# Kernel tuning notes

Measured on AMD Instinct MI355X. Metric: run time of the kernel, lower is better.

Reference implementation:

```python
import jax, jax.numpy as jnp
import numpy as np

NDIM, NINEQ, NEQ = 1024, 512, 256
EPS = 1e-4       # Q regularization (module's eps)
N_ITERS = 25     # fixed primal-dual interior-point iterations
SIGMA = 0.1      # centering parameter


def setup_inputs() -> dict:
    key = jax.random.key(0)
    ks = jax.random.split(key, 5)
    L = jnp.tril(jax.random.uniform(ks[0], (NDIM, NDIM)))                      # tril(rand) as in torch init
    q = jax.random.uniform(ks[1], (NDIM,), minval=-1.0, maxval=1.0)
    G = jax.random.uniform(ks[2], (NINEQ, NDIM), minval=-1.0, maxval=1.0)
    A = jax.random.uniform(ks[3], (NEQ, NDIM), minval=-1.0, maxval=1.0)
    b = jax.random.uniform(ks[4], (NEQ,), minval=-1.0, maxval=1.0)
    x0 = jnp.zeros((NDIM,), jnp.float32)   # nn.Parameter(torch.zeros(ndim))
    s0 = jnp.ones((NINEQ,), jnp.float32)   # nn.Parameter(torch.ones(nineq))
    return {"L": L, "q": q, "G": G, "A": A, "b": b, "x0": x0, "s0": s0}


def _frac_to_boundary(v, dv):
    # max step alpha in (0,1] keeping v + alpha*dv > 0, with 0.99 backoff
    safe_dv = jnp.where(dv < 0, dv, -1.0)
    ratio = jnp.where(dv < 0, -v / safe_dv, 1.0)
    return jnp.min(ratio)


def _solve_qp(Q, q, G, h, A, b):
    n, m, p = q.shape[0], h.shape[0], b.shape[0]

    def step(state, _):
        x, s, z, y = state
        r_x = Q @ x + q + G.T @ z + A.T @ y          # dual residual
        r_p = G @ x + s - h                           # primal ineq residual
        r_y = A @ x - b                               # primal eq residual
        mu = jnp.dot(s, z) / m
        r_c = s * z - SIGMA * mu                      # centered complementarity
        D = z / s                                     # diag scaling
        H = Q + G.T @ (D[:, None] * G)                # reduced Hessian [n,n]
        KKT = jnp.block([[H, A.T], [A, jnp.zeros((p, p), Q.dtype)]])
        rhs = jnp.concatenate([-(r_x + G.T @ ((-r_c + z * r_p) / s)), -r_y])
        sol = jnp.linalg.solve(KKT, rhs)
        dx, dy = sol[:n], sol[n:]
        ds = -r_p - G @ dx
        dz = (-r_c - z * ds) / s
        alpha = 0.99 * jnp.minimum(1.0, jnp.minimum(_frac_to_boundary(s, ds), _frac_to_boundary(z, dz)))
        return (x + alpha * dx, s + alpha * ds, z + alpha * dz, y + alpha * dy), None

    init = (jnp.zeros((n,), Q.dtype), jnp.ones((m,), Q.dtype), jnp.ones((m,), Q.dtype), jnp.zeros((p,), Q.dtype))
    (x, s, z, y), _ = jax.lax.scan(step, init, None, length=N_ITERS)
    return x


def reference(L, q, G, A, b, x0, s0):
    Lt = jnp.tril(L)  # M * L with M = tril(ones)
    Q = Lt @ Lt.T + EPS * jnp.eye(L.shape[0], dtype=L.dtype)
    h = G @ x0 + s0   # learn_h branch (source's self.z0 is self.x0)
    return _solve_qp(Q, q, G, h, A, b)
```

## Files before the change

### kernel.cpp

```cpp
#include <hip/hip_runtime.h>
#include <hip/hip_bf16.h>


constexpr int ND = 1024;
constexpr int MI = 512;
constexpr int PE = 256;
constexpr int NM = 512;
constexpr int LDM = 520;
constexpr double EPSQ = 1e-4;
constexpr double SIG = 0.1;
constexpr int NITER = 25;

__device__ __forceinline__ double wred(double v) {
#pragma unroll
  for (int off = 32; off; off >>= 1) v += __shfl_down(v, off, 64);
  return v;
}

__global__ void k_prep(const float* __restrict__ Gf, const float* __restrict__ Af,
                       const float* __restrict__ qf, const float* __restrict__ bf,
                       float* __restrict__ GTf, float* __restrict__ ATf,
                       double* __restrict__ qd, double* __restrict__ bd,
                       double* __restrict__ xv, double* __restrict__ sv,
                       double* __restrict__ zv, double* __restrict__ yv,
                       double* __restrict__ scal) {
  if (blockIdx.x == 0 && threadIdx.x == 0) { scal[0] = 1.0; scal[1] = 0.0; }
  for (size_t idx = (size_t)blockIdx.x * blockDim.x + threadIdx.x;
       idx < (size_t)MI * ND; idx += (size_t)gridDim.x * blockDim.x) {
    int k = (int)(idx >> 10), i = (int)(idx & 1023);
    GTf[(size_t)i * MI + k] = Gf[idx];
    if (idx < (size_t)PE * ND) ATf[(size_t)i * PE + k] = Af[idx];
    if (idx < ND) { qd[idx] = (double)qf[idx]; xv[idx] = 0.0; }
    if (idx < MI) { sv[idx] = 1.0; zv[idx] = 1.0; }
    if (idx < PE) { bd[idx] = (double)bf[idx]; yv[idx] = 0.0; }
  }
}

__global__ __launch_bounds__(256) void k_h(const float* __restrict__ Gf,
                                           const float* __restrict__ x0f,
                                           const float* __restrict__ s0f,
                                           double* __restrict__ hd) {
  int wid = blockIdx.x * 4 + (int)(threadIdx.x >> 6), lane = threadIdx.x & 63;
  if (wid >= MI) return;
  double acc = 0;
  for (int c = lane; c < ND; c += 64) acc += (double)Gf[(size_t)wid * ND + c] * (double)x0f[c];
  acc = wred(acc);
  if (lane == 0) hd[wid] = acc + (double)s0f[wid];
}

__global__ __launch_bounds__(256) void k_qbuild(const float* __restrict__ Lf,
                                                double* __restrict__ Qd, double* __restrict__ LQ) {
  __shared__ double As[32][33], Bs[32][33];
  int i0 = blockIdx.y * 32, j0 = blockIdx.x * 32;
  int tx = threadIdx.x & 15, ty = threadIdx.x >> 4;
  double acc[2][2] = {};
  int kmax = (i0 < j0 ? i0 : j0) + 32;
  for (int k0 = 0; k0 < kmax; k0 += 32) {
    for (int l = threadIdx.x; l < 1024; l += 256) {
      int r = l >> 5, c = l & 31;
      As[r][c] = (k0 + c <= i0 + r) ? (double)Lf[(size_t)(i0 + r) * ND + k0 + c] : 0.0;
      Bs[r][c] = (k0 + c <= j0 + r) ? (double)Lf[(size_t)(j0 + r) * ND + k0 + c] : 0.0;
    }
    __syncthreads();
#pragma unroll
    for (int k = 0; k < 32; k++) {
      double a0 = As[2 * ty][k], a1 = As[2 * ty + 1][k];
      double b0 = Bs[2 * tx][k], b1 = Bs[2 * tx + 1][k];
      acc[0][0] += a0 * b0; acc[0][1] += a0 * b1;
      acc[1][0] += a1 * b0; acc[1][1] += a1 * b1;
    }
    __syncthreads();
  }
  for (int da = 0; da < 2; da++)
    for (int db = 0; db < 2; db++) {
      int i = i0 + 2 * ty + da, j = j0 + 2 * tx + db;
      double v = acc[da][db] + (i == j ? EPSQ : 0.0);
      Qd[(size_t)i * ND + j] = v;
      LQ[(size_t)i * ND + j] = v;
    }
}

__global__ __launch_bounds__(256) void k_chol_diag_inv(double* __restrict__ A, int lda, int kb,
                                                       double* __restrict__ DG) {
  __shared__ double a[4160];
  __shared__ double invp[2080];
  __shared__ double dtmp[64];
  int t = threadIdx.x;
  size_t base = (size_t)kb * 64;
  for (int l = t; l < 4096; l += 256) { int r = l >> 6, c = l & 63; a[r * 65 + c] = A[(base + r) * lda + base + c]; }
  __syncthreads();
  if (t == 0) {
    double m = 0;
    for (int i = 0; i < 64; i++) m = fmax(m, fabs(a[i * 65 + i]));
    a[4159] = m * 1e-28 + 1e-280;
  }
  __syncthreads();
  double dfl = a[4159];
  int rg = t >> 6, ln = t & 63;
  for (int j = 0; j < 64; ++j) {
    double invd = 1.0 / fmax(a[j * 65 + j], dfl);
    for (int r = j + 1 + rg; r < 64; r += 4) {
      int c = j + 1 + ln;
      if (c <= r) a[r * 65 + c] -= a[r * 65 + j] * a[c * 65 + j] * invd;
    }
    __syncthreads();
  }
  if (t < 64) dtmp[t] = 1.0 / sqrt(fmax(a[t * 65 + t], dfl));
  __syncthreads();
  for (int l = t; l < 4096; l += 256) { int r = l >> 6, c = l & 63; if (c <= r) a[r * 65 + c] *= dtmp[c]; }
  __syncthreads();
  for (int l = t; l < 4096; l += 256) { int r = l >> 6, c = l & 63; if (c <= r) A[(base + r) * lda + base + c] = a[r * 65 + c]; }
  if (t < 64) {
    int c = t;
    for (int i = c; i < 64; i++) {
      double v = (i == c) ? 1.0 : 0.0;
      for (int k = c; k < i; k++) v -= a[i * 65 + k] * invp[k * (k + 1) / 2 + c];
      invp[i * (i + 1) / 2 + c] = v / a[i * 65 + i];
    }
  }
  __syncthreads();
  for (int l = t; l < 4096; l += 256) {
    int r = l >> 6, c = l & 63;
    DG[(size_t)kb * 4096 + (size_t)c * 64 + r] = (c <= r) ? invp[r * (r + 1) / 2 + c] : 0.0;
  }
}

__global__ __launch_bounds__(256) void k_fps2(double* __restrict__ A, int lda,
                                              double* __restrict__ PL, int ldp,
                                              double* __restrict__ DG, int kb, int nbk) {
  extern __shared__ double sh[];
  double* D  = sh;
  double* Cb = sh + 4160;
  double* Pb = sh + 8320;
  double* Lb = sh + 12480;
  const int t = threadIdx.x, tx = t & 15, ty = t >> 4;
  const bool tail = (kb + 2 >= nbk);
  int bi = 0, bj = 0;
  if (!tail) {
    int idx = blockIdx.x;
    bi = (int)((sqrtf(8.0f * (float)idx + 1.0f) - 1.0f) * 0.5f);
    while ((bi + 1) * (bi + 2) / 2 <= idx) ++bi;
    while (bi * (bi + 1) / 2 > idx) --bi;
    bj = idx - bi * (bi + 1) / 2;
  }
  const int ib = kb + 2 + bi, jb = kb + 2 + bj;
  const bool isDiag = (ib == jb);
  const bool isBoss = (blockIdx.x == 0);

  double tmp[4][4];
  auto loadTile = [&](double* dst, int rb, int cb) {
    for (int l = t; l < 4096; l += 256) {
      int r = l >> 6, c = l & 63;
      dst[r * 65 + c] = A[(size_t)(rb * 64 + r) * lda + cb * 64 + c];
    }
  };
  auto mulD = [&](const double* X) {
#pragma unroll
    for (int e = 0; e < 4; e++)
#pragma unroll
      for (int f = 0; f < 4; f++) tmp[e][f] = 0;
    for (int k = 0; k < 64; ++k) {
      double x0 = X[ty * 65 + k], x1 = X[(ty + 16) * 65 + k];
      double x2 = X[(ty + 32) * 65 + k], x3 = X[(ty + 48) * 65 + k];
      double d0 = D[k * 64 + tx], d1 = D[k * 64 + tx + 16];
      double d2 = D[k * 64 + tx + 32], d3 = D[k * 64 + tx + 48];
      tmp[0][0] += x0 * d0; tmp[0][1] += x0 * d1; tmp[0][2] += x0 * d2; tmp[0][3] += x0 * d3;
      tmp[1][0] += x1 * d0; tmp[1][1] += x1 * d1; tmp[1][2] += x1 * d2; tmp[1][3] += x1 * d3;
      tmp[2][0] += x2 * d0; tmp[2][1] += x2 * d1; tmp[2][2] += x2 * d2; tmp[2][3] += x2 * d3;
      tmp[3][0] += x3 * d0; tmp[3][1] += x3 * d1; tmp[3][2] += x3 * d2; tmp[3][3] += x3 * d3;
    }
  };
  auto mulNT = [&](const double* X, const double* Y) {
#pragma unroll
    for (int e = 0; e < 4; e++)
#pragma unroll
      for (int f = 0; f < 4; f++) tmp[e][f] = 0;
    for (int k = 0; k < 64; ++k) {
      double x0 = X[ty * 65 + k], x1 = X[(ty + 16) * 65 + k];
      double x2 = X[(ty + 32) * 65 + k], x3 = X[(ty + 48) * 65 + k];
      double y0 = Y[tx * 65 + k], y1 = Y[(tx + 16) * 65 + k];
      double y2 = Y[(tx + 32) * 65 + k], y3 = Y[(tx + 48) * 65 + k];
      tmp[0][0] += x0 * y0; tmp[0][1] += x0 * y1; tmp[0][2] += x0 * y2; tmp[0][3] += x0 * y3;
      tmp[1][0] += x1 * y0; tmp[1][1] += x1 * y1; tmp[1][2] += x1 * y2; tmp[1][3] += x1 * y3;
      tmp[2][0] += x2 * y0; tmp[2][1] += x2 * y1; tmp[2][2] += x2 * y2; tmp[2][3] += x2 * y3;
      tmp[3][0] += x3 * y0; tmp[3][1] += x3 * y1; tmp[3][2] += x3 * y2; tmp[3][3] += x3 * y3;
    }
  };
  auto storeTmp = [&](double* dst) {
    __syncthreads();
#pragma unroll
    for (int e = 0; e < 4; e++)
#pragma unroll
      for (int f = 0; f < 4; f++) dst[(ty + 16 * e) * 65 + tx + 16 * f] = tmp[e][f];
    __syncthreads();
  };
  auto factorD = [&](int dgout) {
    if (t == 0) {
      double m = 0;
      for (int i2 = 0; i2 < 64; i2++) m = fmax(m, fabs(D[i2 * 65 + i2]));
      D[4159] = m * 1e-28 + 1e-280;
    }
    __syncthreads();
    double dfl = D[4159];
    int rg = t >> 6, ln = t & 63;
    for (int j = 0; j < 64; ++j) {
      double invd = 1.0 / fmax(D[j * 65 + j], dfl);
      for (int r = j + 1 + rg; r < 64; r += 4) {
        int c = j + 1 + ln;
        if (c <= r) D[r * 65 + c] -= D[r * 65 + j] * D[c * 65 + j] * invd;
      }
      __syncthreads();
    }
    double* invp = Cb;
    double* dtmp = Cb + 2080;
    if (t < 64) dtmp[t] = 1.0 / sqrt(fmax(D[t * 65 + t], dfl));
    __syncthreads();
    for (int l = t; l < 4096; l += 256) { int r = l >> 6, c = l & 63; if (c <= r) D[r * 65 + c] *= dtmp[c]; }
    __syncthreads();
    if (t < 64) {
      int c = t;
      for (int i2 = c; i2 < 64; ++i2) {
        double v = (i2 == c) ? 1.0 : 0.0;
        for (int k = c; k < i2; ++k) v -= D[i2 * 65 + k] * invp[k * (k + 1) / 2 + c];
        invp[i2 * (i2 + 1) / 2 + c] = v / D[i2 * 65 + i2];
      }
    }
    __syncthreads();
    for (int l = t; l < 4096; l += 256) {
      int k = l >> 6, c = l & 63;
      D[k * 64 + c] = (k <= c) ? invp[c * (c + 1) / 2 + k] : 0.0;
    }
    __syncthreads();
    if (dgout >= 0 && isBoss)
      for (int l = t; l < 4096; l += 256) DG[(size_t)dgout * 4096 + l] = D[l];
    __syncthreads();
  };

  for (int l = t; l < 4096; l += 256) D[l] = DG[(size_t)kb * 4096 + l];
  __syncthreads();

  if (tail) {
    loadTile(Lb, kb + 1, kb);
    __syncthreads();
    mulD(Lb); storeTmp(Cb);
    for (int l = t; l < 4096; l += 256) {
      int r = l >> 6, c = l & 63;
      PL[(size_t)((kb + 1) * 64 + r) * ldp + kb * 64 + c] = Cb[r * 65 + c];
    }
    mulNT(Cb, Cb);
    __syncthreads();
#pragma unroll
    for (int e = 0; e < 4; e++)
#pragma unroll
      for (int f = 0; f < 4; f++)
        D[(ty + 16 * e) * 65 + tx + 16 * f] =
            A[(size_t)((kb + 1) * 64 + ty + 16 * e) * lda + (kb + 1) * 64 + tx + 16 * f] - tmp[e][f];
    __syncthreads();
    factorD(kb + 1);
    return;
  }

  double acc[4][4];
#pragma unroll
  for (int e = 0; e < 4; e++)
#pragma unroll
    for (int f = 0; f < 4; f++)
      acc[e][f] = A[(size_t)(ib * 64 + ty + 16 * e) * lda + jb * 64 + tx + 16 * f];

  loadTile(Lb, kb + 1, kb);
  __syncthreads();
  mulD(Lb); storeTmp(Cb);
  if (isBoss)
    for (int l = t; l < 4096; l += 256) {
      int r = l >> 6, c = l & 63;
      PL[(size_t)((kb + 1) * 64 + r) * ldp + kb * 64 + c] = Cb[r * 65 + c];
    }
  loadTile(Lb, ib, kb);
  __syncthreads();
  mulD(Lb); storeTmp(Pb);
  if (isDiag)
    for (int l = t; l < 4096; l += 256) {
      int r = l >> 6, c = l & 63;
      PL[(size_t)(ib * 64 + r) * ldp + kb * 64 + c] = Pb[r * 65 + c];
    }
  if (!isDiag) {
    loadTile(Lb, jb, kb);
    __syncthreads();
    mulD(Lb); storeTmp(Lb);
  }
  const double* Pj0 = isDiag ? Pb : Lb;
  mulNT(Pb, Pj0);
#pragma unroll
  for (int e = 0; e < 4; e++)
#pragma unroll
    for (int f = 0; f < 4; f++) acc[e][f] -= tmp[e][f];
  mulNT(Pb, Cb);
#pragma unroll
  for (int e = 0; e < 4; e++)
#pragma unroll
    for (int f = 0; f < 4; f++)
      tmp[e][f] = A[(size_t)(ib * 64 + ty + 16 * e) * lda + (kb + 1) * 64 + tx + 16 * f] - tmp[e][f];
  storeTmp(Pb);
  if (!isDiag) {
    mulNT(Lb, Cb);
#pragma unroll
    for (int e = 0; e < 4; e++)
#pragma unroll
      for (int f = 0; f < 4; f++)
        tmp[e][f] = A[(size_t)(jb * 64 + ty + 16 * e) * lda + (kb + 1) * 64 + tx + 16 * f] - tmp[e][f];
    storeTmp(Lb);
  }
  mulNT(Cb, Cb);
  __syncthreads();
#pragma unroll
  for (int e = 0; e < 4; e++)
#pragma unroll
    for (int f = 0; f < 4; f++)
      D[(ty + 16 * e) * 65 + tx + 16 * f] =
          A[(size_t)((kb + 1) * 64 + ty + 16 * e) * lda + (kb + 1) * 64 + tx + 16 * f] - tmp[e][f];
  __syncthreads();
  factorD(kb + 1);
  mulD(Pb); storeTmp(Pb);
  if (isDiag)
    for (int l = t; l < 4096; l += 256) {
      int r = l >> 6, c = l & 63;
      PL[(size_t)(ib * 64 + r) * ldp + (kb + 1) * 64 + c] = Pb[r * 65 + c];
    }
  if (!isDiag) { mulD(Lb); storeTmp(Lb); }
  const double* Pj1 = isDiag ? Pb : Lb;
  mulNT(Pb, Pj1);
#pragma unroll
  for (int e = 0; e < 4; e++)
#pragma unroll
    for (int f = 0; f < 4; f++) acc[e][f] -= tmp[e][f];

  if (isBoss) {
    __syncthreads();
#pragma unroll
    for (int e = 0; e < 4; e++)
#pragma unroll
      for (int f = 0; f < 4; f++) D[(ty + 16 * e) * 65 + tx + 16 * f] = acc[e][f];
    __syncthreads();
    factorD(kb + 2);
  } else {
#pragma unroll
    for (int e = 0; e < 4; e++)
#pragma unroll
      for (int f = 0; f < 4; f++)
        A[(size_t)(ib * 64 + ty + 16 * e) * lda + jb * 64 + tx + 16 * f] = acc[e][f];
  }
}

__global__ __launch_bounds__(256) void k_trsmf_g(const double* __restrict__ Lm, int lda,
                                                 double* __restrict__ X, int ldx,
                                                 const double* __restrict__ DG, int kb) {
  __shared__ double Lb[64][64];
  __shared__ double Xs[64][33];
  int t = threadIdx.x;
  int c0 = blockIdx.x * 32;
  int lane2 = t & 31, rbase = t >> 5;
  int row0 = kb * 64;
  double acc[8];
#pragma unroll
  for (int e = 0; e < 8; e++) acc[e] = (row0 + rbase + 8 * e == c0 + lane2) ? 1.0 : 0.0;
  for (int jb = 0; jb < kb; jb++) {
    for (int l = t; l < 4096; l += 256) { int r = l >> 6, c = l & 63; Lb[r][c] = Lm[(size_t)(row0 + r) * lda + jb * 64 + c]; }
    for (int l = t; l < 2048; l += 256) { int k = l >> 5, c = l & 31; Xs[k][c] = X[(size_t)(jb * 64 + k) * ldx + c0 + c]; }
    __syncthreads();
#pragma unroll 4
    for (int k = 0; k < 64; k++) {
      double wv = Xs[k][lane2];
#pragma unroll
      for (int e = 0; e < 8; e++) acc[e] -= Lb[rbase + 8 * e][k] * wv;
    }
    __syncthreads();
  }
  __syncthreads();
#pragma unroll
  for (int e = 0; e < 8; e++) Xs[rbase + 8 * e][lane2] = acc[e];
  for (int l = t; l < 4096; l += 256) Lb[l >> 6][l & 63] = DG[(size_t)kb * 4096 + l];
  __syncthreads();
#pragma unroll
  for (int e = 0; e < 8; e++) {
    int i = rbase + 8 * e;
    double s = 0;
#pragma unroll 4
    for (int k = 0; k < 64; k++) s += Lb[k][i] * Xs[k][lane2];
    X[(size_t)(row0 + i) * ldx + c0 + lane2] = s;
  }
}

__global__ __launch_bounds__(256) void k_trsmb_g(const double* __restrict__ Lm, int lda,
                                                 double* __restrict__ X, int ldx,
                                                 const double* __restrict__ DG, int kb, int nkb) {
  __shared__ double Lb[64][64];
  __shared__ double Xs[64][33];
  int t = threadIdx.x;
  int c0 = blockIdx.x * 32;
  int lane2 = t & 31, rbase = t >> 5;
  int row0 = kb * 64;
  double acc[8];
#pragma unroll
  for (int e = 0; e < 8; e++) acc[e] = X[(size_t)(row0 + rbase + 8 * e) * ldx + c0 + lane2];
  for (int jb = kb + 1; jb < nkb; jb++) {
    for (int l = t; l < 4096; l += 256) { int r = l >> 6, c = l & 63; Lb[r][c] = Lm[(size_t)(jb * 64 + r) * lda + kb * 64 + c]; }
    for (int l = t; l < 2048; l += 256) { int k = l >> 5, c = l & 31; Xs[k][c] = X[(size_t)(jb * 64 + k) * ldx + c0 + c]; }
    __syncthreads();
#pragma unroll 4
    for (int k = 0; k < 64; k++) {
      double wv = Xs[k][lane2];
#pragma unroll
      for (int e = 0; e < 8; e++) acc[e] -= Lb[k][rbase + 8 * e] * wv;
    }
    __syncthreads();
  }
  __syncthreads();
#pragma unroll
  for (int e = 0; e < 8; e++) Xs[rbase + 8 * e][lane2] = acc[e];
  for (int l = t; l < 4096; l += 256) Lb[l >> 6][l & 63] = DG[(size_t)kb * 4096 + l];
  __syncthreads();
#pragma unroll
  for (int e = 0; e < 8; e++) {
    int i = rbase + 8 * e;
    double s = 0;
#pragma unroll 4
    for (int k = 0; k < 64; k++) s += Lb[i][k] * Xs[k][lane2];
    X[(size_t)(row0 + i) * ldx + c0 + lane2] = s;
  }
}

__global__ __launch_bounds__(256) void k_aqi(const float* __restrict__ Af, const double* __restrict__ Qi,
                                             double* __restrict__ AQi) {
  __shared__ double As[32][33], Bs[32][33];
  int i0 = blockIdx.x * 32, a0 = blockIdx.y * 32;
  int tx = threadIdx.x & 15, ty = threadIdx.x >> 4;
  double acc[2][2] = {};
  for (int k0 = 0; k0 < ND; k0 += 32) {
    for (int l = threadIdx.x; l < 1024; l += 256) {
      int r = l >> 5, c = l & 31;
      As[r][c] = (double)Af[(size_t)(a0 + r) * ND + k0 + c];
      Bs[r][c] = Qi[(size_t)(k0 + r) * ND + i0 + c];
    }
    __syncthreads();
#pragma unroll
    for (int k = 0; k < 32; k++) {
      double a0v = As[2 * ty][k], a1v = As[2 * ty + 1][k];
      double b0v = Bs[k][2 * tx], b1v = Bs[k][2 * tx + 1];
      acc[0][0] += a0v * b0v; acc[0][1] += a0v * b1v;
      acc[1][0] += a1v * b0v; acc[1][1] += a1v * b1v;
    }
    __syncthreads();
  }
  for (int da = 0; da < 2; da++)
    for (int db = 0; db < 2; db++)
      AQi[(size_t)(a0 + 2 * ty + da) * ND + i0 + 2 * tx + db] = acc[da][db];
}

__global__ __launch_bounds__(256) void k_sa(const double* __restrict__ AQi, const float* __restrict__ Af,
                                            double* __restrict__ SA) {
  __shared__ double As[32][33], Bs[32][33];
  int a0 = blockIdx.y * 32, b0 = blockIdx.x * 32;
  int tx = threadIdx.x & 15, ty = threadIdx.x >> 4;
  double acc[2][2] = {};
  for (int k0 = 0; k0 < ND; k0 += 32) {
    for (int l = threadIdx.x; l < 1024; l += 256) {
      int r = l >> 5, c = l & 31;
      As[r][c] = AQi[(size_t)(a0 + r) * ND + k0 + c];
      Bs[r][c] = (double)Af[(size_t)(b0 + r) * ND + k0 + c];
    }
    __syncthreads();
#pragma unroll
    for (int k = 0; k < 32; k++) {
      double a0v = As[2 * ty][k], a1v = As[2 * ty + 1][k];
      double b0v = Bs[2 * tx][k], b1v = Bs[2 * tx + 1][k];
      acc[0][0] += a0v * b0v; acc[0][1] += a0v * b1v;
      acc[1][0] += a1v * b0v; acc[1][1] += a1v * b1v;
    }
    __syncthreads();
  }
  for (int da = 0; da < 2; da++)
    for (int db = 0; db < 2; db++)
      SA[(size_t)(a0 + 2 * ty + da) * PE + b0 + 2 * tx + db] = acc[da][db];
}

__global__ __launch_bounds__(256) void k_xy(const double* __restrict__ AQi, const double* __restrict__ SAi,
                                            double* __restrict__ XY) {
  __shared__ double As[32][33], Bs[32][33];
  int b0 = blockIdx.x * 32, i0 = blockIdx.y * 32;
  int tx = threadIdx.x & 15, ty = threadIdx.x >> 4;
  double acc[2][2] = {};
  for (int k0 = 0; k0 < PE; k0 += 32) {
    for (int l = threadIdx.x; l < 1024; l += 256) {
      int r = l >> 5, c = l & 31;
      As[r][c] = AQi[(size_t)(k0 + r) * ND + i0 + c];
      Bs[r][c] = SAi[(size_t)(k0 + r) * PE + b0 + c];
    }
    __syncthreads();
#pragma unroll
    for (int k = 0; k < 32; k++) {
      double a0v = As[k][2 * ty], a1v = As[k][2 * ty + 1];
      double b0v = Bs[k][2 * tx], b1v = Bs[k][2 * tx + 1];
      acc[0][0] += a0v * b0v; acc[0][1] += a0v * b1v;
      acc[1][0] += a1v * b0v; acc[1][1] += a1v * b1v;
    }
    __syncthreads();
  }
  for (int da = 0; da < 2; da++)
    for (int db = 0; db < 2; db++)
      XY[(size_t)(i0 + 2 * ty + da) * PE + b0 + 2 * tx + db] = acc[da][db];
}

__global__ __launch_bounds__(256) void k_xx(const double* __restrict__ Qi, const double* __restrict__ XY,
                                            const double* __restrict__ AQi, double* __restrict__ XX) {
  __shared__ double As[32][33], Bs[32][33];
  int j0 = blockIdx.x * 32, i0 = blockIdx.y * 32;
  int tx = threadIdx.x & 15, ty = threadIdx.x >> 4;
  double acc[2][2] = {};
  for (int k0 = 0; k0 < PE; k0 += 32) {
    for (int l = threadIdx.x; l < 1024; l += 256) {
      int r = l >> 5, c = l & 31;
      As[r][c] = XY[(size_t)(i0 + r) * PE + k0 + c];
      Bs[r][c] = AQi[(size_t)(k0 + r) * ND + j0 + c];
    }
    __syncthreads();
#pragma unroll
    for (int k = 0; k < 32; k++) {
      double a0v = As[2 * ty][k], a1v = As[2 * ty + 1][k];
      double b0v = Bs[k][2 * tx], b1v = Bs[k][2 * tx + 1];
      acc[0][0] += a0v * b0v; acc[0][1] += a0v * b1v;
      acc[1][0] += a1v * b0v; acc[1][1] += a1v * b1v;
    }
    __syncthreads();
  }
  for (int da = 0; da < 2; da++)
    for (int db = 0; db < 2; db++) {
      int i = i0 + 2 * ty + da, j = j0 + 2 * tx + db;
      XX[(size_t)i * ND + j] = Qi[(size_t)i * ND + j] - acc[da][db];
    }
}

__global__ __launch_bounds__(256) void k_fk0x(const float* __restrict__ Gf, const double* __restrict__ XX,
                                              double* __restrict__ FK0x) {
  __shared__ double As[32][33], Bs[32][33];
  int j0 = blockIdx.x * 32, g0 = blockIdx.y * 32;
  int tx = threadIdx.x & 15, ty = threadIdx.x >> 4;
  double acc[2][2] = {};
  for (int k0 = 0; k0 < ND; k0 += 32) {
    for (int l = threadIdx.x; l < 1024; l += 256) {
      int r = l >> 5, c = l & 31;
      As[r][c] = (double)Gf[(size_t)(g0 + r) * ND + k0 + c];
      Bs[r][c] = XX[(size_t)(k0 + r) * ND + j0 + c];
    }
    __syncthreads();
#pragma unroll
    for (int k = 0; k < 32; k++) {
      double a0v = As[2 * ty][k], a1v = As[2 * ty + 1][k];
      double b0v = Bs[k][2 * tx], b1v = Bs[k][2 * tx + 1];
      acc[0][0] += a0v * b0v; acc[0][1] += a0v * b1v;
      acc[1][0] += a1v * b0v; acc[1][1] += a1v * b1v;
    }
    __syncthreads();
  }
  for (int da = 0; da < 2; da++)
    for (int db = 0; db < 2; db++)
      FK0x[(size_t)(g0 + 2 * ty + da) * ND + j0 + 2 * tx + db] = acc[da][db];
}

__global__ __launch_bounds__(256) void k_fk0y(const float* __restrict__ Gf, const double* __restrict__ XY,
                                              double* __restrict__ FK0y) {
  __shared__ double As[32][33], Bs[32][33];
  int b0 = blockIdx.x * 32, g0 = blockIdx.y * 32;
  int tx = threadIdx.x & 15, ty = threadIdx.x >> 4;
  double acc[2][2] = {};
  for (int k0 = 0; k0 < ND; k0 += 32) {
    for (int l = threadIdx.x; l < 1024; l += 256) {
      int r = l >> 5, c = l & 31;
      As[r][c] = (double)Gf[(size_t)(g0 + r) * ND + k0 + c];
      Bs[r][c] = XY[(size_t)(k0 + r) * PE + b0 + c];
    }
    __syncthreads();
#pragma unroll
    for (int k = 0; k < 32; k++) {
      double a0v = As[2 * ty][k], a1v = As[2 * ty + 1][k];
      double b0v = Bs[k][2 * tx], b1v = Bs[k][2 * tx + 1];
      acc[0][0] += a0v * b0v; acc[0][1] += a0v * b1v;
      acc[1][0] += a1v * b0v; acc[1][1] += a1v * b1v;
    }
    __syncthreads();
  }
  for (int da = 0; da < 2; da++)
    for (int db = 0; db < 2; db++)
      FK0y[(size_t)(g0 + 2 * ty + da) * PE + b0 + 2 * tx + db] = acc[da][db];
}

__global__ __launch_bounds__(256) void k_smat(const double* __restrict__ FK0x, const float* __restrict__ Gf,
                                              double* __restrict__ S) {
  __shared__ double As[32][33], Bs[32][33];
  int g0 = blockIdx.y * 32, h0 = blockIdx.x * 32;
  int tx = threadIdx.x & 15, ty = threadIdx.x >> 4;
  double acc[2][2] = {};
  for (int k0 = 0; k0 < ND; k0 += 32) {
    for (int l = threadIdx.x; l < 1024; l += 256) {
      int r = l >> 5, c = l & 31;
      As[r][c] = FK0x[(size_t)(g0 + r) * ND + k0 + c];
      Bs[r][c] = (double)Gf[(size_t)(h0 + r) * ND + k0 + c];
    }
    __syncthreads();
#pragma unroll
    for (int k = 0; k < 32; k++) {
      double a0v = As[2 * ty][k], a1v = As[2 * ty + 1][k];
      double b0v = Bs[2 * tx][k], b1v = Bs[2 * tx + 1][k];
      acc[0][0] += a0v * b0v; acc[0][1] += a0v * b1v;
      acc[1][0] += a1v * b0v; acc[1][1] += a1v * b1v;
    }
    __syncthreads();
  }
  for (int da = 0; da < 2; da++)
    for (int db = 0; db < 2; db++)
      S[(size_t)(g0 + 2 * ty + da) * MI + h0 + 2 * tx + db] = acc[da][db];
}

__global__ __launch_bounds__(256) void k_tr(const double* __restrict__ src, double* __restrict__ dst,
                                            int R, int Cc) {
  __shared__ double tile[32][33];
  int r0 = blockIdx.y * 32, c0 = blockIdx.x * 32;
  for (int l = threadIdx.x; l < 1024; l += 256) {
    int r = l >> 5, c = l & 31;
    tile[r][c] = src[(size_t)(r0 + r) * Cc + c0 + c];
  }
  __syncthreads();
  for (int l = threadIdx.x; l < 1024; l += 256) {
    int r = l >> 5, c = l & 31;
    dst[(size_t)(c0 + r) * R + r0 + c] = tile[c][r];
  }
}

__global__ __launch_bounds__(256) void k_A1(const double* __restrict__ Qd, const float* __restrict__ Gf,
                                            const float* __restrict__ Af, const float* __restrict__ GTf,
                                            const float* __restrict__ ATf, const double* __restrict__ qd,
                                            const double* __restrict__ bd, const double* __restrict__ hd,
                                            const double* __restrict__ xv, const double* __restrict__ sv,
                                            const double* __restrict__ zv, const double* __restrict__ yv,
                                            const double* __restrict__ scal, const double* __restrict__ S,
                                            double* __restrict__ rxv, double* __restrict__ rp,
                                            double* __restrict__ ry, double* __restrict__ uv,
                                            double* __restrict__ dinv, double* __restrict__ Mm) {
  int t = threadIdx.x, lane = t & 63;
  if (blockIdx.x < 256) {
    int wid = blockIdx.x * 4 + (t >> 6);
    double acc = 0;
    for (int k = lane; k < ND; k += 64) acc += Qd[(size_t)wid * ND + k] * xv[k];
    for (int k = lane; k < MI; k += 64) acc += (double)GTf[(size_t)wid * MI + k] * zv[k];
    for (int k = lane; k < PE; k += 64) acc += (double)ATf[(size_t)wid * PE + k] * yv[k];
    acc = wred(acc);
    if (lane == 0) rxv[wid] = acc + qd[wid];
  } else if (blockIdx.x < 448) {
    int wid = (blockIdx.x - 256) * 4 + (t >> 6);
    if (wid < MI) {
      double acc = 0;
      for (int c = lane; c < ND; c += 64) acc += (double)Gf[(size_t)wid * ND + c] * xv[c];
      acc = wred(acc);
      if (lane == 0) {
        double s0 = sv[wid], z0 = zv[wid];
        double rpv = acc + s0 - hd[wid];
        rp[wid] = rpv;
        double rc0 = s0 * z0 - SIG * scal[0];
        uv[wid] = (-rc0 + z0 * rpv) / s0;
        dinv[wid] = s0 / z0;
      }
    } else {
      int r = wid - MI;
      double acc = 0;
      for (int c = lane; c < ND; c += 64) acc += (double)Af[(size_t)r * ND + c] * xv[c];
      acc = wred(acc);
      if (lane == 0) ry[r] = acc - bd[r];
    }
  } else {
    int rbase = (blockIdx.x - 448) * 8;
    for (int rr = 0; rr < 8; ++rr) {
      int row = rbase + rr;
      for (int c = t; c < NM; c += 256) {
        double v = S[(size_t)row * MI + c];
        if (row == c) v += sv[row] / zv[row];
        Mm[(size_t)row * LDM + c] = v;
      }
    }
  }
}

__global__ __launch_bounds__(256) void k_A2(const double* __restrict__ rxv, const float* __restrict__ GTf,
                                            const double* __restrict__ uv, const double* __restrict__ ry,
                                            const double* __restrict__ S, const double* __restrict__ FK0x,
                                            const double* __restrict__ FK0y, double* __restrict__ rhs1,
                                            double* __restrict__ Mm, double* __restrict__ DGC) {
  __shared__ double sh2[6304];
  int t = threadIdx.x, lane = t & 63;
  if (blockIdx.x < 256) {
    int wid = blockIdx.x * 4 + (t >> 6);
    double acc = 0;
    for (int k = lane; k < MI; k += 64) acc += (double)GTf[(size_t)wid * MI + k] * uv[k];
    acc = wred(acc);
    if (lane == 0) rhs1[wid] = -(rxv[wid] + acc);
  } else if (blockIdx.x < 384) {
    int j = (blockIdx.x - 256) * 4 + (t >> 6);
    double acc = 0;
    for (int k = lane; k < ND; k += 64) acc += FK0x[(size_t)j * ND + k] * rxv[k];
    for (int m = lane; m < MI; m += 64) acc += S[(size_t)j * MI + m] * uv[m];
    for (int c = lane; c < PE; c += 64) acc += FK0y[(size_t)j * PE + c] * ry[c];
    acc = wred(acc);
    if (lane == 0) Mm[(size_t)NM * LDM + j] = -acc;
  } else {
    double* a = sh2;
    double* invp = sh2 + 4160;
    double* dtmp = sh2 + 6240;
    for (int l = t; l < 4096; l += 256) { int r = l >> 6, c = l & 63; a[r * 65 + c] = Mm[(size_t)r * LDM + c]; }
    __syncthreads();
    if (t == 0) {
      double m = 0;
      for (int i = 0; i < 64; i++) m = fmax(m, fabs(a[i * 65 + i]));
      a[4159] = m * 1e-28 + 1e-280;
    }
    __syncthreads();
    double dfl = a[4159];
    int rg = t >> 6, ln = t & 63;
    for (int j = 0; j < 64; ++j) {
      double invd = 1.0 / fmax(a[j * 65 + j], dfl);
      for (int r = j + 1 + rg; r < 64; r += 4) {
        int c = j + 1 + ln;
        if (c <= r) a[r * 65 + c] -= a[r * 65 + j] * a[c * 65 + j] * invd;
      }
      __syncthreads();
    }
    if (t < 64) dtmp[t] = 1.0 / sqrt(fmax(a[t * 65 + t], dfl));
    __syncthreads();
    for (int l = t; l < 4096; l += 256) { int r = l >> 6, c = l & 63; if (c <= r) a[r * 65 + c] *= dtmp[c]; }
    __syncthreads();
    if (t < 64) {
      int c = t;
      for (int i = c; i < 64; i++) {
        double v = (i == c) ? 1.0 : 0.0;
        for (int k = c; k < i; k++) v -= a[i * 65 + k] * invp[k * (k + 1) / 2 + c];
        invp[i * (i + 1) / 2 + c] = v / a[i * 65 + i];
      }
    }
    __syncthreads();
    for (int l = t; l < 4096; l += 256) {
      int r = l >> 6, c = l & 63;
      DGC[(size_t)c * 64 + r] = (c <= r) ? invp[r * (r + 1) / 2 + c] : 0.0;
    }
  }
}

__global__ __launch_bounds__(512) void k_bwdupd(const double* __restrict__ Mm, const double* __restrict__ PL,
                                                const double* __restrict__ DGC, const double* __restrict__ rp,
                                                const double* __restrict__ dinv, double* __restrict__ sv,
                                                double* __restrict__ zv, double* __restrict__ scal,
                                                double* __restrict__ solw) {
  __shared__ double DT[4096];
  __shared__ double g[NM];
  __shared__ double pseg[64];
  __shared__ double acc8[8][64];
  __shared__ double tmp[64];
  __shared__ double red[512];
  __shared__ double dsA[512];
  __shared__ double dzA[512];
  int t = threadIdx.x;
  for (int l = t; l < NM; l += 512) g[l] = Mm[(size_t)NM * LDM + l];
  for (int kbp = 0; kbp < 8; ++kbp) {
    __syncthreads();
    for (int l = t; l < 4096; l += 512) DT[l] = DGC[(size_t)kbp * 4096 + l];
    __syncthreads();
    if (t < 64) {
      double s = 0;
#pragma unroll
      for (int k = 0; k < 64; k++) s += g[kbp * 64 + k] * DT[k * 64 + t];
      pseg[t] = s;
    }
    __syncthreads();
    for (int c = (kbp + 1) * 64 + t; c < NM; c += 512) {
      double s = 0;
#pragma unroll
      for (int k = 0; k < 64; k++) s += pseg[k] * PL[(size_t)c * NM + kbp * 64 + k];
      g[c] -= s;
    }
    if (t < 64) g[kbp * 64 + t] = pseg[t];
  }
  int i8 = t & 63, p8 = t >> 6;
  for (int kb = 7; kb >= 0; --kb) {
    __syncthreads();
    for (int l = t; l < 4096; l += 512) DT[l] = DGC[(size_t)kb * 4096 + l];
    __syncthreads();
    int tr0 = kb * 64 + 64;
    double s = 0;
    for (int rr = p8; rr < NM - tr0; rr += 8)
      s += PL[(size_t)(tr0 + rr) * NM + kb * 64 + i8] * g[tr0 + rr];
    acc8[p8][i8] = s;
    __syncthreads();
    if (t < 64) {
      double v = g[kb * 64 + t];
#pragma unroll
      for (int p = 0; p < 8; p++) v -= acc8[p][t];
      tmp[t] = v;
    }
    __syncthreads();
    if (t < 64) {
      double v = 0;
#pragma unroll
      for (int l = 0; l < 64; l++) v += DT[t * 64 + l] * tmp[l];
      pseg[t] = v;
    }
    __syncthreads();
    if (t < 64) g[kb * 64 + t] = pseg[t];
  }
  __syncthreads();
  solw[t] = g[t];
  double mu = scal[0];
  double s0 = sv[t], z0 = zv[t];
  double ds = -rp[t] - dinv[t] * g[t];
  double rc0 = s0 * z0 - SIG * mu;
  double dz = (-rc0 - z0 * ds) / s0;
  dsA[t] = ds; dzA[t] = dz;
  double rs = (ds < 0.0) ? -s0 / ds : 1.0;
  double rz = (dz < 0.0) ? -z0 / dz : 1.0;
  red[t] = fmin(rs, rz);
  __syncthreads();
  for (int s2 = 256; s2; s2 >>= 1) { if (t < s2) red[t] = fmin(red[t], red[t + s2]); __syncthreads(); }
  double alpha = 0.99 * fmin(1.0, red[0]);
  if (!(alpha == alpha)) alpha = 0.0;
  double us = alpha * dsA[t], uz = alpha * dzA[t];
  if (isfinite(us)) sv[t] += us;
  if (isfinite(uz)) zv[t] += uz;
  __syncthreads();
  red[t] = sv[t] * zv[t];
  __syncthreads();
  for (int s2 = 256; s2; s2 >>= 1) { if (t < s2) red[t] += red[t + s2]; __syncthreads(); }
  if (t == 0) { scal[0] = red[0] / (double)MI; scal[1] = alpha; }
}

__global__ __launch_bounds__(256) void k_C(const double* __restrict__ XX, const double* __restrict__ XGT,
                                           const double* __restrict__ XY, const double* __restrict__ YXm,
                                           const double* __restrict__ YGT, const double* __restrict__ SAi,
                                           const double* __restrict__ rhs1, const double* __restrict__ solw,
                                           const double* __restrict__ ry, const double* __restrict__ scal,
                                           double* __restrict__ xv, double* __restrict__ yv) {
  int lane = threadIdx.x & 63;
  double al = scal[1];
  if (blockIdx.x < 256) {
    int wid = blockIdx.x * 4 + (int)(threadIdx.x >> 6);
    double acc = 0;
    for (int k = lane; k < ND; k += 64) acc += XX[(size_t)wid * ND + k] * rhs1[k];
    for (int m = lane; m < MI; m += 64) acc -= XGT[(size_t)wid * MI + m] * solw[m];
    for (int c = lane; c < PE; c += 64) acc -= XY[(size_t)wid * PE + c] * ry[c];
    acc = wred(acc);
    if (lane == 0) { double u = al * acc; if (isfinite(u)) xv[wid] += u; }
  } else {
    int r = (blockIdx.x - 256) * 4 + (int)(threadIdx.x >> 6);
    double acc = 0;
    for (int k = lane; k < ND; k += 64) acc += YXm[(size_t)r * ND + k] * rhs1[k];
    for (int m = lane; m < MI; m += 64) acc -= YGT[(size_t)r * MI + m] * solw[m];
    for (int c = lane; c < PE; c += 64) acc += SAi[(size_t)r * PE + c] * ry[c];
    acc = wred(acc);
    if (lane == 0) { double u = al * acc; if (isfinite(u)) yv[r] += u; }
  }
}

__global__ void k_out(const double* __restrict__ xv, float* __restrict__ out) {
  int i = blockIdx.x * blockDim.x + threadIdx.x;
  if (i < ND) out[i] = (float)xv[i];
}

__global__ void k_wsdiag(float mb, float* out) {
  int i = blockIdx.x * 256 + threadIdx.x;
  if (i < ND) out[i] = (i == 0 ? (65536.0f * (1.0f + mb)) : 0.0f);
}

extern "C" void kernel_launch(void* const* d_in, const int* in_sizes, int n_in,
                              void* d_out, int out_size, void* d_ws, size_t ws_size,
                              hipStream_t stream) {
  const float* Lf = (const float*)d_in[0];
  const float* qf = (const float*)d_in[1];
  const float* Gf = (const float*)d_in[2];
  const float* Af = (const float*)d_in[3];
  const float* bf = (const float*)d_in[4];
  const float* x0f = (const float*)d_in[5];
  const float* s0f = (const float*)d_in[6];

  double* w = (double*)d_ws;
  double* Qd  = w; w += (size_t)ND * ND;
  double* XX  = w; w += (size_t)ND * ND;
  double* R1  = w; w += (size_t)ND * ND;
  double* R2  = w; w += (size_t)ND * ND;
  double* XY  = w; w += (size_t)ND * PE;
  double* FK0xReg = w; w += (size_t)MI * ND;
  double* SA  = w; w += (size_t)PE * PE;
  double* PLi = w; w += (size_t)NM * NM;
  double* DGH = w; w += (size_t)16 * 4096;
  double* DGA = w; w += (size_t)4 * 4096;
  double* DGC = w; w += (size_t)8 * 4096;
  double* qd = w; w += ND;  double* bd = w; w += PE;  double* hd = w; w += MI;
  double* xv = w; w += ND;  double* sv = w; w += MI;  double* zv = w; w += MI;  double* yv = w; w += PE;
  double* rxv = w; w += ND; double* rp = w; w += MI;  double* ry = w; w += PE;
  double* uv = w; w += MI;  double* dinv = w; w += MI;
  double* rhs1 = w; w += ND; double* solw = w; w += NM;
  double* scal = w; w += 16;
  float* GTf = (float*)w;
  float* ATf = GTf + (size_t)ND * MI;
  char* wend = (char*)(ATf + (size_t)ND * PE);
  size_t need = (size_t)(wend - (char*)d_ws);
  if (ws_size < need) {
    k_wsdiag<<<4, 256, 0, stream>>>((float)(ws_size >> 20), (float*)d_out);
    return;
  }

  double* Qi  = R1;
  double* XGT = R1;
  double* YXm = R1 + (size_t)ND * MI;
  double* YGT = R1 + (size_t)ND * MI + (size_t)PE * ND;
  double* LQ  = R2;
  double* Mm  = R2;
  double* FK0y = R2 + (size_t)(NM + 1) * LDM;
  double* SAi  = FK0y + (size_t)MI * PE;
  double* Smat = SAi + (size_t)PE * PE;
  double* AQi  = FK0xReg;
  double* FK0x = FK0xReg;
  double* PLQ  = XX;
  double* PLA  = XY;

  const size_t ldsFPS = (size_t)16640 * sizeof(double);

  k_prep<<<2048, 256, 0, stream>>>(Gf, Af, qf, bf, GTf, ATf, qd, bd, xv, sv, zv, yv, scal);
  k_h<<<128, 256, 0, stream>>>(Gf, x0f, s0f, hd);
  { dim3 g(32, 32); k_qbuild<<<g, 256, 0, stream>>>(Lf, Qd, LQ); }
  k_chol_diag_inv<<<1, 256, 0, stream>>>(LQ, ND, 0, DGH);
  for (int kb = 0; kb < 16; kb += 2) {
    int T = 16 - kb - 2;
    int grid = (T > 0) ? T * (T + 1) / 2 : 1;
    k_fps2<<<grid, 256, ldsFPS, stream>>>(LQ, ND, PLQ, ND, DGH, kb, 16);
  }
  for (int kb = 0; kb < 16; kb++)  k_trsmf_g<<<32, 256, 0, stream>>>(PLQ, ND, Qi, ND, DGH, kb);
  for (int kb = 15; kb >= 0; kb--) k_trsmb_g<<<32, 256, 0, stream>>>(PLQ, ND, Qi, ND, DGH, kb, 16);
  { dim3 g(32, 8);  k_aqi<<<g, 256, 0, stream>>>(Af, Qi, AQi); }
  { dim3 g(8, 8);   k_sa<<<g, 256, 0, stream>>>(AQi, Af, SA); }
  k_chol_diag_inv<<<1, 256, 0, stream>>>(SA, PE, 0, DGA);
  for (int kb = 0; kb < 4; kb += 2) {
    int T = 4 - kb - 2;
    int grid = (T > 0) ? T * (T + 1) / 2 : 1;
    k_fps2<<<grid, 256, ldsFPS, stream>>>(SA, PE, PLA, PE, DGA, kb, 4);
  }
  for (int kb = 0; kb < 4; kb++)  k_trsmf_g<<<8, 256, 0, stream>>>(PLA, PE, SAi, PE, DGA, kb);
  for (int kb = 3; kb >= 0; kb--) k_trsmb_g<<<8, 256, 0, stream>>>(PLA, PE, SAi, PE, DGA, kb, 4);
  { dim3 g(8, 32);  k_xy<<<g, 256, 0, stream>>>(AQi, SAi, XY); }
  { dim3 g(32, 32); k_xx<<<g, 256, 0, stream>>>(Qi, XY, AQi, XX); }
  { dim3 g(32, 16); k_fk0x<<<g, 256, 0, stream>>>(Gf, XX, FK0x); }
  { dim3 g(8, 16);  k_fk0y<<<g, 256, 0, stream>>>(Gf, XY, FK0y); }
  { dim3 g(16, 16); k_smat<<<g, 256, 0, stream>>>(FK0x, Gf, Smat); }
  { dim3 g(32, 16); k_tr<<<g, 256, 0, stream>>>(FK0x, XGT, MI, ND); }
  { dim3 g(8, 32);  k_tr<<<g, 256, 0, stream>>>(XY, YXm, ND, PE); }
  { dim3 g(8, 16);  k_tr<<<g, 256, 0, stream>>>(FK0y, YGT, MI, PE); }

  for (int it = 0; it < NITER; ++it) {
    k_A1<<<512, 256, 0, stream>>>(Qd, Gf, Af, GTf, ATf, qd, bd, hd, xv, sv, zv, yv, scal,
                                  Smat, rxv, rp, ry, uv, dinv, Mm);
    k_A2<<<385, 256, 0, stream>>>(rxv, GTf, uv, ry, Smat, FK0x, FK0y, rhs1, Mm, DGC);
    for (int kb = 0; kb < 8; kb += 2) {
      int T = 8 - kb - 2;
      int grid = (T > 0) ? T * (T + 1) / 2 : 1;
      k_fps2<<<grid, 256, ldsFPS, stream>>>(Mm, LDM, PLi, NM, DGC, kb, 8);
    }
    k_bwdupd<<<1, 512, 0, stream>>>(Mm, PLi, DGC, rp, dinv, sv, zv, scal, solw);
    k_C<<<320, 256, 0, stream>>>(XX, XGT, XY, YXm, YGT, SAi, rhs1, solw, ry, scal, xv, yv);
  }
  k_out<<<4, 256, 0, stream>>>(xv, (float*)d_out);
}
```

Baseline: 36.69 ms.

## Fuse tail Cholesky panels and solve into one single-block kernel

Replaces the last two k_fps2 launches of the per-iteration 512x512 blocked Cholesky and the separate backward/update kernel with a single one-block kernel, k_tailsolve. That kernel factors block columns 4-7 in shared memory (panel multiply, trailing update, diagonal factor and inverse), then runs the forward/backward solve and the step update. The aim is to cut launch overhead and inter-kernel gaps in the latency-bound iteration loop, at the cost of running the small trailing updates on one workgroup serially.

```diff
diff --git a/kernel.cpp b/kernel.cpp
--- a/kernel.cpp
+++ b/kernel.cpp
@@ -751,33 +751,173 @@
   }
 }
 
-__global__ __launch_bounds__(512) void k_bwdupd(const double* __restrict__ Mm, const double* __restrict__ PL,
-                                                const double* __restrict__ DGC, const double* __restrict__ rp,
-                                                const double* __restrict__ dinv, double* __restrict__ sv,
-                                                double* __restrict__ zv, double* __restrict__ scal,
-                                                double* __restrict__ solw) {
-  __shared__ double DT[4096];
-  __shared__ double g[NM];
-  __shared__ double pseg[64];
-  __shared__ double acc8[8][64];
-  __shared__ double tmp[64];
-  __shared__ double red[512];
-  __shared__ double dsA[512];
-  __shared__ double dzA[512];
-  int t = threadIdx.x;
-  for (int l = t; l < NM; l += 512) g[l] = Mm[(size_t)NM * LDM + l];
+__global__ __launch_bounds__(256) void k_tailsolve(double* __restrict__ Mm, double* __restrict__ PL,
+                                                   double* __restrict__ DGC, const double* __restrict__ rp,
+                                                   const double* __restrict__ dinv, double* __restrict__ sv,
+                                                   double* __restrict__ zv, double* __restrict__ scal,
+                                                   double* __restrict__ solw) {
+  extern __shared__ double sh[];
+  double* D = sh;
+  double* U = sh + 4160;
+  double* V = sh + 8320;
+  const int t = threadIdx.x, tx = t & 15, ty = t >> 4;
+  double tmp[4][4];
+
+  auto mulD = [&](const double* X) {
+#pragma unroll
+    for (int e = 0; e < 4; e++)
+#pragma unroll
+      for (int f = 0; f < 4; f++) tmp[e][f] = 0;
+    for (int k = 0; k < 64; ++k) {
+      double x0 = X[ty * 65 + k], x1 = X[(ty + 16) * 65 + k];
+      double x2 = X[(ty + 32) * 65 + k], x3 = X[(ty + 48) * 65 + k];
+      double d0 = D[k * 64 + tx], d1 = D[k * 64 + tx + 16];
+      double d2 = D[k * 64 + tx + 32], d3 = D[k * 64 + tx + 48];
+      tmp[0][0] += x0 * d0; tmp[0][1] += x0 * d1; tmp[0][2] += x0 * d2; tmp[0][3] += x0 * d3;
+      tmp[1][0] += x1 * d0; tmp[1][1] += x1 * d1; tmp[1][2] += x1 * d2; tmp[1][3] += x1 * d3;
+      tmp[2][0] += x2 * d0; tmp[2][1] += x2 * d1; tmp[2][2] += x2 * d2; tmp[2][3] += x2 * d3;
+      tmp[3][0] += x3 * d0; tmp[3][1] += x3 * d1; tmp[3][2] += x3 * d2; tmp[3][3] += x3 * d3;
+    }
+  };
+  auto mulNT = [&](const double* X, const double* Y) {
+#pragma unroll
+    for (int e = 0; e < 4; e++)
+#pragma unroll
+      for (int f = 0; f < 4; f++) tmp[e][f] = 0;
+    for (int k = 0; k < 64; ++k) {
+      double x0 = X[ty * 65 + k], x1 = X[(ty + 16) * 65 + k];
+      double x2 = X[(ty + 32) * 65 + k], x3 = X[(ty + 48) * 65 + k];
+      double y0 = Y[tx * 65 + k], y1 = Y[(tx + 16) * 65 + k];
+      double y2 = Y[(tx + 32) * 65 + k], y3 = Y[(tx + 48) * 65 + k];
+      tmp[0][0] += x0 * y0; tmp[0][1] += x0 * y1; tmp[0][2] += x0 * y2; tmp[0][3] += x0 * y3;
+      tmp[1][0] += x1 * y0; tmp[1][1] += x1 * y1; tmp[1][2] += x1 * y2; tmp[1][3] += x1 * y3;
+      tmp[2][0] += x2 * y0; tmp[2][1] += x2 * y1; tmp[2][2] += x2 * y2; tmp[2][3] += x2 * y3;
+      tmp[3][0] += x3 * y0; tmp[3][1] += x3 * y1; tmp[3][2] += x3 * y2; tmp[3][3] += x3 * y3;
+    }
+  };
+  auto storeTmp = [&](double* dst) {
+    __syncthreads();
+#pragma unroll
+    for (int e = 0; e < 4; e++)
+#pragma unroll
+      for (int f = 0; f < 4; f++) dst[(ty + 16 * e) * 65 + tx + 16 * f] = tmp[e][f];
+    __syncthreads();
+  };
+  auto factorD = [&](int dgout) {
+    if (t == 0) {
+      double m = 0;
+      for (int i2 = 0; i2 < 64; i2++) m = fmax(m, fabs(D[i2 * 65 + i2]));
+      D[4159] = m * 1e-28 + 1e-280;
+    }
+    __syncthreads();
+    double dfl = D[4159];
+    int rg = t >> 6, ln = t & 63;
+    for (int j = 0; j < 64; ++j) {
+      double invd = 1.0 / fmax(D[j * 65 + j], dfl);
+      for (int r = j + 1 + rg; r < 64; r += 4) {
+        int c = j + 1 + ln;
+        if (c <= r) D[r * 65 + c] -= D[r * 65 + j] * D[c * 65 + j] * invd;
+      }
+      __syncthreads();
+    }
+    double* invp = U;
+    double* dtmp = U + 2080;
+    if (t < 64) dtmp[t] = 1.0 / sqrt(fmax(D[t * 65 + t], dfl));
+    __syncthreads();
+    for (int l = t; l < 4096; l += 256) { int r = l >> 6, c = l & 63; if (c <= r) D[r * 65 + c] *= dtmp[c]; }
+    __syncthreads();
+    if (t < 64) {
+      int c = t;
+      for (int i2 = c; i2 < 64; ++i2) {
+        double v = (i2 == c) ? 1.0 : 0.0;
+        for (int k = c; k < i2; ++k) v -= D[i2 * 65 + k] * invp[k * (k + 1) / 2 + c];
+        invp[i2 * (i2 + 1) / 2 + c] = v / D[i2 * 65 + i2];
+      }
+    }
+    __syncthreads();
+    for (int l = t; l < 4096; l += 256) {
+      int k = l >> 6, c = l & 63;
+      D[k * 64 + c] = (k <= c) ? invp[c * (c + 1) / 2 + k] : 0.0;
+    }
+    __syncthreads();
+    for (int l = t; l < 4096; l += 256) DGC[(size_t)dgout * 4096 + l] = D[l];
+    __syncthreads();
+  };
+
+  for (int l = t; l < 4096; l += 256) D[l] = DGC[(size_t)4 * 4096 + l];
+  __syncthreads();
+  for (int kb = 4; kb <= 6; ++kb) {
+    for (int i = kb + 1; i <= 7; ++i) {
+      for (int l = t; l < 4096; l += 256) {
+        int r = l >> 6, c = l & 63;
+        U[r * 65 + c] = Mm[(size_t)(i * 64 + r) * LDM + kb * 64 + c];
+      }
+      __syncthreads();
+      mulD(U); storeTmp(U);
+      for (int l = t; l < 4096; l += 256) {
+        int r = l >> 6, c = l & 63;
+        PL[(size_t)(i * 64 + r) * NM + kb * 64 + c] = U[r * 65 + c];
+      }
+      __syncthreads();
+    }
+    __threadfence_block();
+    __syncthreads();
+    for (int i = 7; i >= kb + 1; --i)
+      for (int j = i; j >= kb + 1; --j) {
+        for (int l = t; l < 4096; l += 256) {
+          int r = l >> 6, c = l & 63;
+          U[r * 65 + c] = PL[(size_t)(i * 64 + r) * NM + kb * 64 + c];
+        }
+        if (j != i)
+          for (int l = t; l < 4096; l += 256) {
+            int r = l >> 6, c = l & 63;
+            V[r * 65 + c] = PL[(size_t)(j * 64 + r) * NM + kb * 64 + c];
+          }
+        __syncthreads();
+        mulNT(U, (j == i) ? U : V);
+        if (i == kb + 1 && j == kb + 1) {
+          __syncthreads();
+#pragma unroll
+          for (int e = 0; e < 4; e++)
+#pragma unroll
+            for (int f = 0; f < 4; f++)
+              D[(ty + 16 * e) * 65 + tx + 16 * f] =
+                  Mm[(size_t)(i * 64 + ty + 16 * e) * LDM + j * 64 + tx + 16 * f] - tmp[e][f];
+          __syncthreads();
+        } else {
+#pragma unroll
+          for (int e = 0; e < 4; e++)
+#pragma unroll
+            for (int f = 0; f < 4; f++)
+              Mm[(size_t)(i * 64 + ty + 16 * e) * LDM + j * 64 + tx + 16 * f] -= tmp[e][f];
+          __syncthreads();
+        }
+      }
+    factorD(kb + 1);
+  }
+
+  double* DTs = sh;
+  double* g   = sh + 4160;
+  double* pseg = sh + 4672;
+  double* acc4 = sh + 4736;
+  double* tmp2 = sh + 4992;
+  double* red  = sh + 5056;
+  double* dsA  = sh + 5568;
+  double* dzA  = sh + 6080;
+  __syncthreads();
+  for (int l = t; l < NM; l += 256) g[l] = Mm[(size_t)NM * LDM + l];
   for (int kbp = 0; kbp < 8; ++kbp) {
     __syncthreads();
-    for (int l = t; l < 4096; l += 512) DT[l] = DGC[(size_t)kbp * 4096 + l];
+    for (int l = t; l < 4096; l += 256) DTs[l] = DGC[(size_t)kbp * 4096 + l];
     __syncthreads();
     if (t < 64) {
       double s = 0;
 #pragma unroll
-      for (int k = 0; k < 64; k++) s += g[kbp * 64 + k] * DT[k * 64 + t];
+      for (int k = 0; k < 64; k++) s += g[kbp * 64 + k] * DTs[k * 64 + t];
       pseg[t] = s;
     }
     __syncthreads();
-    for (int c = (kbp + 1) * 64 + t; c < NM; c += 512) {
+    for (int c = (kbp + 1) * 64 + t; c < NM; c += 256) {
       double s = 0;
 #pragma unroll
       for (int k = 0; k < 64; k++) s += pseg[k] * PL[(size_t)c * NM + kbp * 64 + k];
@@ -785,28 +925,23 @@
     }
     if (t < 64) g[kbp * 64 + t] = pseg[t];
   }
-  int i8 = t & 63, p8 = t >> 6;
+  int i4 = t & 63, p4 = t >> 6;
   for (int kb = 7; kb >= 0; --kb) {
     __syncthreads();
-    for (int l = t; l < 4096; l += 512) DT[l] = DGC[(size_t)kb * 4096 + l];
+    for (int l = t; l < 4096; l += 256) DTs[l] = DGC[(size_t)kb * 4096 + l];
     __syncthreads();
     int tr0 = kb * 64 + 64;
     double s = 0;
-    for (int rr = p8; rr < NM - tr0; rr += 8)
-      s += PL[(size_t)(tr0 + rr) * NM + kb * 64 + i8] * g[tr0 + rr];
-    acc8[p8][i8] = s;
-    __syncthreads();
-    if (t < 64) {
-      double v = g[kb * 64 + t];
-#pragma unroll
-      for (int p = 0; p < 8; p++) v -= acc8[p][t];
-      tmp[t] = v;
-    }
+    for (int rr = p4; rr < NM - tr0; rr += 4)
+      s += PL[(size_t)(tr0 + rr) * NM + kb * 64 + i4] * g[tr0 + rr];
+    acc4[p4 * 64 + i4] = s;
+    __syncthreads();
+    if (t < 64) tmp2[t] = g[kb * 64 + t] - (acc4[t] + acc4[64 + t] + acc4[128 + t] + acc4[192 + t]);
     __syncthreads();
     if (t < 64) {
       double v = 0;
 #pragma unroll
-      for (int l = 0; l < 64; l++) v += DT[t * 64 + l] * tmp[l];
+      for (int l2 = 0; l2 < 64; l2++) v += DTs[t * 64 + l2] * tmp2[l2];
       pseg[t] = v;
     }
     __syncthreads();
@@ -814,24 +949,32 @@
   }
   __syncthreads();
   solw[t] = g[t];
+  solw[t + 256] = g[t + 256];
   double mu = scal[0];
-  double s0 = sv[t], z0 = zv[t];
-  double ds = -rp[t] - dinv[t] * g[t];
-  double rc0 = s0 * z0 - SIG * mu;
-  double dz = (-rc0 - z0 * ds) / s0;
-  dsA[t] = ds; dzA[t] = dz;
-  double rs = (ds < 0.0) ? -s0 / ds : 1.0;
-  double rz = (dz < 0.0) ? -z0 / dz : 1.0;
-  red[t] = fmin(rs, rz);
+  for (int e = 0; e < 2; ++e) {
+    int id = t + 256 * e;
+    double s0 = sv[id], z0 = zv[id];
+    double ds = -rp[id] - dinv[id] * g[id];
+    double rc0 = s0 * z0 - SIG * mu;
+    double dz = (-rc0 - z0 * ds) / s0;
+    dsA[id] = ds; dzA[id] = dz;
+    double rs = (ds < 0.0) ? -s0 / ds : 1.0;
+    double rz = (dz < 0.0) ? -z0 / dz : 1.0;
+    red[id] = fmin(rs, rz);
+  }
   __syncthreads();
   for (int s2 = 256; s2; s2 >>= 1) { if (t < s2) red[t] = fmin(red[t], red[t + s2]); __syncthreads(); }
   double alpha = 0.99 * fmin(1.0, red[0]);
   if (!(alpha == alpha)) alpha = 0.0;
-  double us = alpha * dsA[t], uz = alpha * dzA[t];
-  if (isfinite(us)) sv[t] += us;
-  if (isfinite(uz)) zv[t] += uz;
+  for (int e = 0; e < 2; ++e) {
+    int id = t + 256 * e;
+    double us = alpha * dsA[id], uz = alpha * dzA[id];
+    if (isfinite(us)) sv[id] += us;
+    if (isfinite(uz)) zv[id] += uz;
+  }
   __syncthreads();
   red[t] = sv[t] * zv[t];
+  red[t + 256] = sv[t + 256] * zv[t + 256];
   __syncthreads();
   for (int s2 = 256; s2; s2 >>= 1) { if (t < s2) red[t] += red[t + s2]; __syncthreads(); }
   if (t == 0) { scal[0] = red[0] / (double)MI; scal[1] = alpha; }
@@ -927,6 +1070,7 @@
   double* PLA  = XY;
 
   const size_t ldsFPS = (size_t)16640 * sizeof(double);
+  const size_t ldsTS  = (size_t)12480 * sizeof(double);
 
   k_prep<<<2048, 256, 0, stream>>>(Gf, Af, qf, bf, GTf, ATf, qd, bd, xv, sv, zv, yv, scal);
   k_h<<<128, 256, 0, stream>>>(Gf, x0f, s0f, hd);
@@ -962,12 +1106,9 @@
     k_A1<<<512, 256, 0, stream>>>(Qd, Gf, Af, GTf, ATf, qd, bd, hd, xv, sv, zv, yv, scal,
                                   Smat, rxv, rp, ry, uv, dinv, Mm);
     k_A2<<<385, 256, 0, stream>>>(rxv, GTf, uv, ry, Smat, FK0x, FK0y, rhs1, Mm, DGC);
-    for (int kb = 0; kb < 8; kb += 2) {
-      int T = 8 - kb - 2;
-      int grid = (T > 0) ? T * (T + 1) / 2 : 1;
-      k_fps2<<<grid, 256, ldsFPS, stream>>>(Mm, LDM, PLi, NM, DGC, kb, 8);
-    }
-    k_bwdupd<<<1, 512, 0, stream>>>(Mm, PLi, DGC, rp, dinv, sv, zv, scal, solw);
+    k_fps2<<<21, 256, ldsFPS, stream>>>(Mm, LDM, PLi, NM, DGC, 0, 8);
+    k_fps2<<<10, 256, ldsFPS, stream>>>(Mm, LDM, PLi, NM, DGC, 2, 8);
+    k_tailsolve<<<1, 256, ldsTS, stream>>>(Mm, PLi, DGC, rp, dinv, sv, zv, scal, solw);
     k_C<<<320, 256, 0, stream>>>(XX, XGT, XY, YXm, YGT, SAi, rhs1, solw, ry, scal, xv, yv);
   }
   k_out<<<4, 256, 0, stream>>>(xv, (float*)d_out);
```

Result: slower. 44.45 ms (+21.2%).
